# Kernel tuning notes

Measured on AMD Instinct MI355X. Metric: run time of the kernel, lower is better.

The kernel has to match this reference:

```python
import math
import jax, jax.numpy as jnp
import numpy as np

B, H, S, D = 2, 16, 2048, 1024
DK = D // H  # 64


def setup_inputs() -> dict:
    key = jax.random.key(0)
    k1, k2, k3, k4, k5 = jax.random.split(key, 5)
    scale = np.float32(0.02)
    return {
        "x": jax.random.normal(k1, (B, H, S, D), dtype=jnp.float32),
        "wq": jax.random.normal(k2, (DK, D), dtype=jnp.float32) * scale,
        "wk": jax.random.normal(k3, (DK, D), dtype=jnp.float32) * scale,
        "wv": jax.random.normal(k4, (DK, D), dtype=jnp.float32) * scale,
        "wo": jax.random.normal(k5, (D, D), dtype=jnp.float32) * scale,
    }


def reference(x, wq, wk, wv, wo):
    # x: [B, H, S, D]; wq/wk/wv: [dk, D]; wo: [D, D]
    b, h, s, d = x.shape
    xq = jnp.einsum("bhsd,kd->bhsk", x, wq)  # [B,H,S,dk]
    xk = jnp.einsum("bhsd,kd->bhsk", x, wk)
    xv = jnp.einsum("bhsd,kd->bhsk", x, wv)
    # NOTE: original scales by sqrt(hidden_dim), not sqrt(dk)
    inv_scale = np.float32(1.0 / math.sqrt(d))
    score = jnp.einsum("bhsk,bhtk->bhst", xq, xk) * inv_scale  # [B,H,S,S]
    attn = jax.nn.softmax(score, axis=-1).astype(xq.dtype)
    out = jnp.einsum("bhst,bhtk->bhsk", attn, xv)  # [B,H,S,dk]
    out = out.transpose(0, 2, 1, 3).reshape(b, s, h * (wq.shape[0]))  # [B,S,H*dk]
    return out @ wo.T  # [B,S,D]
```

## Files before the change

### kernel.cpp

```cpp
#include <hip/hip_runtime.h>
#include <math.h>

#define BB 2
#define HH 16
#define SS 2048
#define DD 1024
#define DK 64
#define BHS (BB*HH*SS)
#define INV_SCALE 0.03125f

typedef short  bf16x8  __attribute__((ext_vector_type(8)));
typedef float  floatx4 __attribute__((ext_vector_type(4)));
typedef unsigned short u16;

#define MFMA(a,b,c) __builtin_amdgcn_mfma_f32_16x16x32_bf16((a),(b),(c),0,0,0)

__device__ __forceinline__ u16 f2bf(float f) {
    union { float f; unsigned u; } v; v.f = f;
    unsigned r = v.u + 0x7FFFu + ((v.u >> 16) & 1u);
    return (u16)(r >> 16);
}
__device__ __forceinline__ bf16x8 ldfrag(const u16* p) {
    union { uint4 u; bf16x8 b; } c;
    c.u = *(const uint4*)p;
    return c.b;
}
__device__ __forceinline__ void stbf4(u16* p, float4 t) {
    union { u16 s[4]; uint2 u; } c;
    c.s[0] = f2bf(t.x); c.s[1] = f2bf(t.y); c.s[2] = f2bf(t.z); c.s[3] = f2bf(t.w);
    *(uint2*)p = c.u;
}

__global__ __launch_bounds__(256) void qkv_proj(
    const float* __restrict__ x,
    const float* __restrict__ wq, const float* __restrict__ wk,
    const float* __restrict__ wv,
    u16* __restrict__ q, u16* __restrict__ k, u16* __restrict__ vT)
{
    __shared__ __align__(16) u16 Xs[64][72];
    __shared__ __align__(16) u16 Ws[192][72];
    const int tid  = threadIdx.x;
    const int w    = tid >> 6;
    const int lane = tid & 63;
    const int quad = lane >> 4;
    const int l16  = lane & 15;
    const int rowbase = blockIdx.x * 64;

    floatx4 acc[12];
#pragma unroll
    for (int n = 0; n < 12; ++n) acc[n] = (floatx4){0.f,0.f,0.f,0.f};

    for (int k0 = 0; k0 < DD; k0 += 64) {
#pragma unroll
        for (int it = 0; it < 4; ++it) {
            int li = tid + it * 256;
            int r  = li >> 4;
            int c4 = li & 15;
            float4 t = *(const float4*)(x + (size_t)(rowbase + r) * DD + k0 + c4 * 4);
            stbf4(&Xs[r][c4 * 4], t);
        }
#pragma unroll
        for (int it = 0; it < 12; ++it) {
            int li = tid + it * 256;
            int r  = li >> 4;
            int c4 = li & 15;
            const float* wsrc = (r < 64) ? wq : ((r < 128) ? wk : wv);
            float4 t = *(const float4*)(wsrc + (size_t)(r & 63) * DD + k0 + c4 * 4);
            stbf4(&Ws[r][c4 * 4], t);
        }
        __syncthreads();

        bf16x8 a0 = ldfrag(&Xs[w * 16 + l16][quad * 8]);
        bf16x8 a1 = ldfrag(&Xs[w * 16 + l16][32 + quad * 8]);
#pragma unroll
        for (int n = 0; n < 12; ++n) {
            bf16x8 b0 = ldfrag(&Ws[n * 16 + l16][quad * 8]);
            bf16x8 b1 = ldfrag(&Ws[n * 16 + l16][32 + quad * 8]);
            acc[n] = MFMA(a0, b0, acc[n]);
            acc[n] = MFMA(a1, b1, acc[n]);
        }
        __syncthreads();
    }

#pragma unroll
    for (int r = 0; r < 4; ++r) {
        int row = w * 16 + quad * 4 + r;
        size_t m = (size_t)(rowbase + row);
#pragma unroll
        for (int n = 0; n < 4; ++n)
            q[m * DK + n * 16 + l16] = f2bf(acc[n][r]);
#pragma unroll
        for (int n = 4; n < 8; ++n)
            k[m * DK + (n - 4) * 16 + l16] = f2bf(acc[n][r]);
    }
    u16 (*Vbuf)[72] = Xs;
#pragma unroll
    for (int r = 0; r < 4; ++r) {
        int row = w * 16 + quad * 4 + r;
#pragma unroll
        for (int n = 8; n < 12; ++n)
            Vbuf[row][(n - 8) * 16 + l16] = f2bf(acc[n][r]);
    }
    __syncthreads();
    {
        const int dk = tid >> 2;
        const int sc = (tid & 3) * 16;
        const int bh = rowbase >> 11;
        const int s0 = rowbase & 2047;
        union { u16 s[16]; uint4 u[2]; } t;
#pragma unroll
        for (int u = 0; u < 16; ++u) t.s[u] = Vbuf[sc + u][dk];
        uint4* dst = (uint4*)(vT + ((size_t)(bh * DK + dk)) * SS + s0 + sc);
        dst[0] = t.u[0];
        dst[1] = t.u[1];
    }
}

__global__ __launch_bounds__(256) void flash_attn(
    const u16* __restrict__ q, const u16* __restrict__ k,
    const u16* __restrict__ vT, u16* __restrict__ ao)
{
    __shared__ __align__(16) u16 Qs[64][72];
    __shared__ __align__(16) u16 Ks[64][72];
    __shared__ __align__(16) u16 Vt[64][72];
    __shared__ __align__(16) u16 Ps[4][16][72];
    const int tid  = threadIdx.x;
    const int w    = tid >> 6;
    const int lane = tid & 63;
    const int quad = lane >> 4;
    const int l16  = lane & 15;
    const int qt   = blockIdx.x;
    const int bh   = blockIdx.y;
    const size_t kbase = (size_t)bh * SS * DK;
    const size_t vbase = (size_t)bh * DK * SS;

#pragma unroll
    for (int it = 0; it < 2; ++it) {
        int li = tid + it * 256;
        int r  = li >> 3;
        int c8 = li & 7;
        *(uint4*)&Qs[r][c8 * 8] =
            *(const uint4*)(q + kbase + (size_t)(qt * 64 + r) * DK + c8 * 8);
    }

    float m_i[4], l_i[4];
    floatx4 acc_o[4];
#pragma unroll
    for (int r = 0; r < 4; ++r) { m_i[r] = -INFINITY; l_i[r] = 0.f; }
#pragma unroll
    for (int n = 0; n < 4; ++n) acc_o[n] = (floatx4){0.f,0.f,0.f,0.f};
    __syncthreads();

    for (int kt = 0; kt < SS / 64; ++kt) {
#pragma unroll
        for (int it = 0; it < 2; ++it) {
            int li = tid + it * 256;
            int r  = li >> 3;
            int c8 = li & 7;
            *(uint4*)&Ks[r][c8 * 8] =
                *(const uint4*)(k + kbase + (size_t)(kt * 64 + r) * DK + c8 * 8);
            *(uint4*)&Vt[r][c8 * 8] =
                *(const uint4*)(vT + vbase + (size_t)r * SS + kt * 64 + c8 * 8);
        }
        __syncthreads();

        floatx4 sc[4];
        {
            bf16x8 a0 = ldfrag(&Qs[w * 16 + l16][quad * 8]);
            bf16x8 a1 = ldfrag(&Qs[w * 16 + l16][32 + quad * 8]);
#pragma unroll
            for (int n = 0; n < 4; ++n) {
                sc[n] = (floatx4){0.f,0.f,0.f,0.f};
                bf16x8 b0 = ldfrag(&Ks[n * 16 + l16][quad * 8]);
                bf16x8 b1 = ldfrag(&Ks[n * 16 + l16][32 + quad * 8]);
                sc[n] = MFMA(a0, b0, sc[n]);
                sc[n] = MFMA(a1, b1, sc[n]);
            }
        }

        float alpha[4];
#pragma unroll
        for (int r = 0; r < 4; ++r) {
            float s0 = sc[0][r] * INV_SCALE, s1 = sc[1][r] * INV_SCALE;
            float s2 = sc[2][r] * INV_SCALE, s3 = sc[3][r] * INV_SCALE;
            float rm = fmaxf(fmaxf(s0, s1), fmaxf(s2, s3));
#pragma unroll
            for (int off = 1; off < 16; off <<= 1)
                rm = fmaxf(rm, __shfl_xor(rm, off, 64));
            float mnew = fmaxf(m_i[r], rm);
            alpha[r] = __expf(m_i[r] - mnew);
            float p0 = __expf(s0 - mnew), p1 = __expf(s1 - mnew);
            float p2 = __expf(s2 - mnew), p3 = __expf(s3 - mnew);
            float rs = (p0 + p1) + (p2 + p3);
#pragma unroll
            for (int off = 1; off < 16; off <<= 1)
                rs += __shfl_xor(rs, off, 64);
            l_i[r] = l_i[r] * alpha[r] + rs;
            m_i[r] = mnew;
            sc[0][r] = p0; sc[1][r] = p1; sc[2][r] = p2; sc[3][r] = p3;
        }

#pragma unroll
        for (int n = 0; n < 4; ++n) {
#pragma unroll
            for (int r = 0; r < 4; ++r) acc_o[n][r] *= alpha[r];
#pragma unroll
            for (int r = 0; r < 4; ++r)
                Ps[w][quad * 4 + r][n * 16 + l16] = f2bf(sc[n][r]);
        }

#pragma unroll
        for (int kc = 0; kc < 2; ++kc) {
            bf16x8 a = ldfrag(&Ps[w][l16][kc * 32 + quad * 8]);
#pragma unroll
            for (int n = 0; n < 4; ++n) {
                bf16x8 b = ldfrag(&Vt[n * 16 + l16][kc * 32 + quad * 8]);
                acc_o[n] = MFMA(a, b, acc_o[n]);
            }
        }
        __syncthreads();
    }

    const int b = bh >> 4, h = bh & 15;
#pragma unroll
    for (int r = 0; r < 4; ++r) {
        int srow = qt * 64 + w * 16 + quad * 4 + r;
        float rl = 1.0f / l_i[r];
        size_t base = ((size_t)(b * SS + srow)) * (HH * DK) + h * 64;
#pragma unroll
        for (int n = 0; n < 4; ++n)
            ao[base + n * 16 + l16] = f2bf(acc_o[n][r] * rl);
    }
}

__global__ __launch_bounds__(256) void out_proj(
    const u16* __restrict__ ao, const float* __restrict__ wo,
    float* __restrict__ out)
{
    __shared__ __align__(16) u16 As[64][72];
    __shared__ __align__(16) u16 Bs[64][72];
    const int tid  = threadIdx.x;
    const int w    = tid >> 6;
    const int lane = tid & 63;
    const int quad = lane >> 4;
    const int l16  = lane & 15;
    const int mt = blockIdx.y;
    const int nt = blockIdx.x;

    floatx4 acc[4];
#pragma unroll
    for (int n = 0; n < 4; ++n) acc[n] = (floatx4){0.f,0.f,0.f,0.f};

    for (int k0 = 0; k0 < DD; k0 += 64) {
#pragma unroll
        for (int it = 0; it < 2; ++it) {
            int li = tid + it * 256;
            int r  = li >> 3;
            int c8 = li & 7;
            *(uint4*)&As[r][c8 * 8] =
                *(const uint4*)(ao + (size_t)(mt * 64 + r) * DD + k0 + c8 * 8);
        }
#pragma unroll
        for (int it = 0; it < 4; ++it) {
            int li = tid + it * 256;
            int r  = li >> 4;
            int c4 = li & 15;
            float4 t = *(const float4*)(wo + (size_t)(nt * 64 + r) * DD + k0 + c4 * 4);
            stbf4(&Bs[r][c4 * 4], t);
        }
        __syncthreads();

        bf16x8 a0 = ldfrag(&As[w * 16 + l16][quad * 8]);
        bf16x8 a1 = ldfrag(&As[w * 16 + l16][32 + quad * 8]);
#pragma unroll
        for (int n = 0; n < 4; ++n) {
            bf16x8 b0 = ldfrag(&Bs[n * 16 + l16][quad * 8]);
            bf16x8 b1 = ldfrag(&Bs[n * 16 + l16][32 + quad * 8]);
            acc[n] = MFMA(a0, b0, acc[n]);
            acc[n] = MFMA(a1, b1, acc[n]);
        }
        __syncthreads();
    }

#pragma unroll
    for (int r = 0; r < 4; ++r) {
        int row = mt * 64 + w * 16 + quad * 4 + r;
#pragma unroll
        for (int n = 0; n < 4; ++n)
            out[(size_t)row * DD + nt * 64 + n * 16 + l16] = acc[n][r];
    }
}

extern "C" void kernel_launch(void* const* d_in, const int* in_sizes, int n_in,
                              void* d_out, int out_size, void* d_ws, size_t ws_size,
                              hipStream_t stream) {
    const float* x  = (const float*)d_in[0];
    const float* wq = (const float*)d_in[1];
    const float* wk = (const float*)d_in[2];
    const float* wv = (const float*)d_in[3];
    const float* wo = (const float*)d_in[4];
    float* out = (float*)d_out;

    u16* q  = (u16*)d_ws;
    u16* k  = q  + (size_t)BHS * DK;
    u16* vT = k  + (size_t)BHS * DK;
    u16* ao = vT + (size_t)BHS * DK;

    qkv_proj<<<dim3(BHS / 64), dim3(256), 0, stream>>>(x, wq, wk, wv, q, k, vT);
    flash_attn<<<dim3(SS / 64, BB * HH), dim3(256), 0, stream>>>(q, k, vT, ao);
    out_proj<<<dim3(DD / 64, (BB * SS) / 64), dim3(256), 0, stream>>>(ao, wo, out);
}
```

Baseline: 584.1 us.

## Pre-convert weights to bf16, fold softmax scale into Q, add lazy rescaling

Adds a kernel that converts the weights to bf16 once per call, so the projection kernels load bf16 weights directly instead of converting fp32 tiles in every block. The softmax scale and log2(e) are folded into Q at projection time, so the attention kernel can use exp2. The running-max rescale is skipped unless the new max exceeds the old one by more than 8. It also uses hardware packed bf16 conversion and rcp, and raises wave priority around the MFMA sections. The lazy rescale lets intermediate values grow up to 2^8 and changes rounding slightly.

Measured after the change: 574.6 us. About the same (-1.6%).

```diff
diff --git a/kernel.cpp b/kernel.cpp
--- a/kernel.cpp
+++ b/kernel.cpp
@@ -7,7 +7,7 @@
 #define DD 1024
 #define DK 64
 #define BHS (BB*HH*SS)
-#define INV_SCALE 0.03125f
+#define QSCALE 0.04508422f
 
 typedef short  bf16x8  __attribute__((ext_vector_type(8)));
 typedef float  floatx4 __attribute__((ext_vector_type(4)));
@@ -15,10 +15,10 @@
 
 #define MFMA(a,b,c) __builtin_amdgcn_mfma_f32_16x16x32_bf16((a),(b),(c),0,0,0)
 
-__device__ __forceinline__ u16 f2bf(float f) {
-    union { float f; unsigned u; } v; v.f = f;
-    unsigned r = v.u + 0x7FFFu + ((v.u >> 16) & 1u);
-    return (u16)(r >> 16);
+__device__ __forceinline__ unsigned cvt_pk_bf16(float lo, float hi) {
+    unsigned r;
+    asm("v_cvt_pk_bf16_f32 %0, %1, %2" : "=v"(r) : "v"(lo), "v"(hi));
+    return r;
 }
 __device__ __forceinline__ bf16x8 ldfrag(const u16* p) {
     union { uint4 u; bf16x8 b; } c;
@@ -26,15 +26,40 @@
     return c.b;
 }
 __device__ __forceinline__ void stbf4(u16* p, float4 t) {
-    union { u16 s[4]; uint2 u; } c;
-    c.s[0] = f2bf(t.x); c.s[1] = f2bf(t.y); c.s[2] = f2bf(t.z); c.s[3] = f2bf(t.w);
-    *(uint2*)p = c.u;
+    union { unsigned u[2]; uint2 v; } c;
+    c.u[0] = cvt_pk_bf16(t.x, t.y);
+    c.u[1] = cvt_pk_bf16(t.z, t.w);
+    *(uint2*)p = c.v;
+}
+__device__ __forceinline__ void st4s(u16* p, float a, float b, float c, float d) {
+    unsigned x = cvt_pk_bf16(a, b), y = cvt_pk_bf16(c, d);
+    p[0]  = (u16)x; p[16] = (u16)(x >> 16);
+    p[32] = (u16)y; p[48] = (u16)(y >> 16);
+}
+
+#define WQKV_CHUNKS (192*1024/4)
+#define WO_CHUNKS   (1024*1024/4)
+__global__ __launch_bounds__(256) void convert_w(
+    const float* __restrict__ wq, const float* __restrict__ wk,
+    const float* __restrict__ wv, const float* __restrict__ wo,
+    u16* __restrict__ wqkv, u16* __restrict__ wo_bf)
+{
+    int i = blockIdx.x * 256 + threadIdx.x;
+    if (i < WQKV_CHUNKS) {
+        int r = i >> 8;
+        int c = i & 255;
+        const float* src = (r < 64) ? wq : ((r < 128) ? wk : wv);
+        float4 t = *(const float4*)(src + (size_t)(r & 63) * DD + c * 4);
+        stbf4(wqkv + (size_t)r * DD + c * 4, t);
+    } else if (i < WQKV_CHUNKS + WO_CHUNKS) {
+        int j = i - WQKV_CHUNKS;
+        float4 t = *(const float4*)(wo + (size_t)j * 4);
+        stbf4(wo_bf + (size_t)j * 4, t);
+    }
 }
 
 __global__ __launch_bounds__(256) void qkv_proj(
-    const float* __restrict__ x,
-    const float* __restrict__ wq, const float* __restrict__ wk,
-    const float* __restrict__ wv,
+    const float* __restrict__ x, const u16* __restrict__ wqkv,
     u16* __restrict__ q, u16* __restrict__ k, u16* __restrict__ vT)
 {
     __shared__ __align__(16) u16 Xs[64][72];
@@ -60,13 +85,12 @@
             stbf4(&Xs[r][c4 * 4], t);
         }
 #pragma unroll
-        for (int it = 0; it < 12; ++it) {
+        for (int it = 0; it < 6; ++it) {
             int li = tid + it * 256;
-            int r  = li >> 4;
-            int c4 = li & 15;
-            const float* wsrc = (r < 64) ? wq : ((r < 128) ? wk : wv);
-            float4 t = *(const float4*)(wsrc + (size_t)(r & 63) * DD + k0 + c4 * 4);
-            stbf4(&Ws[r][c4 * 4], t);
+            int r  = li >> 3;
+            int c8 = li & 7;
+            *(uint4*)&Ws[r][c8 * 8] =
+                *(const uint4*)(wqkv + (size_t)r * DD + k0 + c8 * 8);
         }
         __syncthreads();
 
@@ -86,20 +110,15 @@
     for (int r = 0; r < 4; ++r) {
         int row = w * 16 + quad * 4 + r;
         size_t m = (size_t)(rowbase + row);
-#pragma unroll
-        for (int n = 0; n < 4; ++n)
-            q[m * DK + n * 16 + l16] = f2bf(acc[n][r]);
-#pragma unroll
-        for (int n = 4; n < 8; ++n)
-            k[m * DK + (n - 4) * 16 + l16] = f2bf(acc[n][r]);
+        st4s(&q[m * DK + l16], acc[0][r] * QSCALE, acc[1][r] * QSCALE,
+                               acc[2][r] * QSCALE, acc[3][r] * QSCALE);
+        st4s(&k[m * DK + l16], acc[4][r], acc[5][r], acc[6][r], acc[7][r]);
     }
     u16 (*Vbuf)[72] = Xs;
 #pragma unroll
     for (int r = 0; r < 4; ++r) {
         int row = w * 16 + quad * 4 + r;
-#pragma unroll
-        for (int n = 8; n < 12; ++n)
-            Vbuf[row][(n - 8) * 16 + l16] = f2bf(acc[n][r]);
+        st4s(&Vbuf[row][l16], acc[8][r], acc[9][r], acc[10][r], acc[11][r]);
     }
     __syncthreads();
     {
@@ -165,6 +184,7 @@
         __syncthreads();
 
         floatx4 sc[4];
+        __builtin_amdgcn_s_setprio(1);
         {
             bf16x8 a0 = ldfrag(&Qs[w * 16 + l16][quad * 8]);
             bf16x8 a1 = ldfrag(&Qs[w * 16 + l16][32 + quad * 8]);
@@ -177,38 +197,46 @@
                 sc[n] = MFMA(a1, b1, sc[n]);
             }
         }
-
-        float alpha[4];
+        __builtin_amdgcn_s_setprio(0);
+
+        float rmx[4];
 #pragma unroll
         for (int r = 0; r < 4; ++r) {
-            float s0 = sc[0][r] * INV_SCALE, s1 = sc[1][r] * INV_SCALE;
-            float s2 = sc[2][r] * INV_SCALE, s3 = sc[3][r] * INV_SCALE;
-            float rm = fmaxf(fmaxf(s0, s1), fmaxf(s2, s3));
+            float rm = fmaxf(fmaxf(sc[0][r], sc[1][r]), fmaxf(sc[2][r], sc[3][r]));
 #pragma unroll
             for (int off = 1; off < 16; off <<= 1)
                 rm = fmaxf(rm, __shfl_xor(rm, off, 64));
-            float mnew = fmaxf(m_i[r], rm);
-            alpha[r] = __expf(m_i[r] - mnew);
-            float p0 = __expf(s0 - mnew), p1 = __expf(s1 - mnew);
-            float p2 = __expf(s2 - mnew), p3 = __expf(s3 - mnew);
+            rmx[r] = rm;
+        }
+        int ok = (rmx[0] <= m_i[0] + 8.f) & (rmx[1] <= m_i[1] + 8.f) &
+                 (rmx[2] <= m_i[2] + 8.f) & (rmx[3] <= m_i[3] + 8.f);
+        if (!__all(ok)) {
+#pragma unroll
+            for (int r = 0; r < 4; ++r) {
+                float mnew  = fmaxf(m_i[r], rmx[r]);
+                float alpha = __builtin_amdgcn_exp2f(m_i[r] - mnew);
+#pragma unroll
+                for (int n = 0; n < 4; ++n) acc_o[n][r] *= alpha;
+                l_i[r] *= alpha;
+                m_i[r]  = mnew;
+            }
+        }
+#pragma unroll
+        for (int r = 0; r < 4; ++r) {
+            float mi = m_i[r];
+            float p0 = __builtin_amdgcn_exp2f(sc[0][r] - mi);
+            float p1 = __builtin_amdgcn_exp2f(sc[1][r] - mi);
+            float p2 = __builtin_amdgcn_exp2f(sc[2][r] - mi);
+            float p3 = __builtin_amdgcn_exp2f(sc[3][r] - mi);
             float rs = (p0 + p1) + (p2 + p3);
 #pragma unroll
             for (int off = 1; off < 16; off <<= 1)
                 rs += __shfl_xor(rs, off, 64);
-            l_i[r] = l_i[r] * alpha[r] + rs;
-            m_i[r] = mnew;
-            sc[0][r] = p0; sc[1][r] = p1; sc[2][r] = p2; sc[3][r] = p3;
-        }
-
-#pragma unroll
-        for (int n = 0; n < 4; ++n) {
-#pragma unroll
-            for (int r = 0; r < 4; ++r) acc_o[n][r] *= alpha[r];
-#pragma unroll
-            for (int r = 0; r < 4; ++r)
-                Ps[w][quad * 4 + r][n * 16 + l16] = f2bf(sc[n][r]);
-        }
-
+            l_i[r] += rs;
+            st4s(&Ps[w][quad * 4 + r][l16], p0, p1, p2, p3);
+        }
+
+        __builtin_amdgcn_s_setprio(1);
 #pragma unroll
         for (int kc = 0; kc < 2; ++kc) {
             bf16x8 a = ldfrag(&Ps[w][l16][kc * 32 + quad * 8]);
@@ -218,6 +246,7 @@
                 acc_o[n] = MFMA(a, b, acc_o[n]);
             }
         }
+        __builtin_amdgcn_s_setprio(0);
         __syncthreads();
     }
 
@@ -225,16 +254,15 @@
 #pragma unroll
     for (int r = 0; r < 4; ++r) {
         int srow = qt * 64 + w * 16 + quad * 4 + r;
-        float rl = 1.0f / l_i[r];
+        float rl = __builtin_amdgcn_rcpf(l_i[r]);
         size_t base = ((size_t)(b * SS + srow)) * (HH * DK) + h * 64;
-#pragma unroll
-        for (int n = 0; n < 4; ++n)
-            ao[base + n * 16 + l16] = f2bf(acc_o[n][r] * rl);
+        st4s(&ao[base + l16], acc_o[0][r] * rl, acc_o[1][r] * rl,
+                              acc_o[2][r] * rl, acc_o[3][r] * rl);
     }
 }
 
 __global__ __launch_bounds__(256) void out_proj(
-    const u16* __restrict__ ao, const float* __restrict__ wo,
+    const u16* __restrict__ ao, const u16* __restrict__ wo_bf,
     float* __restrict__ out)
 {
     __shared__ __align__(16) u16 As[64][72];
@@ -259,14 +287,8 @@
             int c8 = li & 7;
             *(uint4*)&As[r][c8 * 8] =
                 *(const uint4*)(ao + (size_t)(mt * 64 + r) * DD + k0 + c8 * 8);
-        }
-#pragma unroll
-        for (int it = 0; it < 4; ++it) {
-            int li = tid + it * 256;
-            int r  = li >> 4;
-            int c4 = li & 15;
-            float4 t = *(const float4*)(wo + (size_t)(nt * 64 + r) * DD + k0 + c4 * 4);
-            stbf4(&Bs[r][c4 * 4], t);
+            *(uint4*)&Bs[r][c8 * 8] =
+                *(const uint4*)(wo_bf + (size_t)(nt * 64 + r) * DD + k0 + c8 * 8);
         }
         __syncthreads();
 
@@ -301,12 +323,16 @@
     const float* wo = (const float*)d_in[4];
     float* out = (float*)d_out;
 
-    u16* q  = (u16*)d_ws;
-    u16* k  = q  + (size_t)BHS * DK;
-    u16* vT = k  + (size_t)BHS * DK;
-    u16* ao = vT + (size_t)BHS * DK;
-
-    qkv_proj<<<dim3(BHS / 64), dim3(256), 0, stream>>>(x, wq, wk, wv, q, k, vT);
+    u16* q    = (u16*)d_ws;
+    u16* k    = q    + (size_t)BHS * DK;
+    u16* vT   = k    + (size_t)BHS * DK;
+    u16* ao   = vT   + (size_t)BHS * DK;
+    u16* wqkv = ao   + (size_t)BHS * DK;
+    u16* wo_bf = wqkv + (size_t)192 * DD;
+
+    convert_w<<<dim3((WQKV_CHUNKS + WO_CHUNKS) / 256), dim3(256), 0, stream>>>(
+        wq, wk, wv, wo, wqkv, wo_bf);
+    qkv_proj<<<dim3(BHS / 64), dim3(256), 0, stream>>>(x, wqkv, q, k, vT);
     flash_attn<<<dim3(SS / 64, BB * HH), dim3(256), 0, stream>>>(q, k, vT, ao);
-    out_proj<<<dim3(DD / 64, (BB * SS) / 64), dim3(256), 0, stream>>>(ao, wo, out);
-}
+    out_proj<<<dim3(DD / 64, (BB * SS) / 64), dim3(256), 0, stream>>>(ao, wo_bf, out);
+}
```
